# Kernel optimization log

Measured on AMD Instinct MI355X. Metric: run time of the kernel, lower is better.

Reference implementation:

```python
import jax, jax.numpy as jnp
import numpy as np
import math

CHUNK = 64

def _linear(x, W, b):
    # torch nn.Linear: y = x @ W.T + b
    return jnp.einsum('bsd,ed->bse', x, W) + b

def setup_inputs() -> dict:
    key = jax.random.key(0)
    ks = jax.random.split(key, 10)
    B, S, D = 4, 4096, 512
    scale = 0.02
    inp = {
        'x': jax.random.normal(ks[0], (B, S, D), jnp.float32),
        'base_phases': jax.random.normal(ks[1], (S, D), jnp.float32) * math.pi,
        'Wk': jax.random.normal(ks[2], (D, D), jnp.float32) * scale,
        'bk': jnp.zeros((D,), jnp.float32),
        'Wv': jax.random.normal(ks[3], (D, D), jnp.float32) * scale,
        'bv': jnp.zeros((D,), jnp.float32),
        'Wq': jax.random.normal(ks[4], (D, D), jnp.float32) * scale,
        'bq': jnp.zeros((D,), jnp.float32),
        'Wkm': jax.random.normal(ks[5], (D, D), jnp.float32) * scale,
        'bkm': jnp.zeros((D,), jnp.float32),
        'Wqm': jax.random.normal(ks[6], (D, D), jnp.float32) * scale,
        'bqm': jnp.zeros((D,), jnp.float32),
        'mod_scale': jnp.ones((1,), jnp.float32) * 0.1,
        'ln_g': jnp.ones((D,), jnp.float32),
        'ln_b': jnp.zeros((D,), jnp.float32),
        'Wo': jax.random.normal(ks[7], (D, D), jnp.float32) * scale,
        'bo': jnp.zeros((D,), jnp.float32),
    }
    return inp

def reference(x, base_phases, Wk, bk, Wv, bv, Wq, bq, Wkm, bkm, Wqm, bqm, mod_scale, ln_g, ln_b, Wo, bo):
    B, S, D = x.shape
    bp = base_phases[:S][None]                      # [1,S,D]
    key = _linear(x, Wk, bk)
    value = _linear(x, Wv, bv)
    query = _linear(x, Wq, bq)
    key_phase = bp + _linear(key, Wkm, bkm) * mod_scale
    query_phase = bp + _linear(query, Wqm, bqm) * mod_scale
    bound_real = value * jnp.cos(key_phase)
    bound_imag = value * jnp.sin(key_phase)
    # chunked cumulative memory (S divisible by CHUNK -> no padding)
    nC = S // CHUNK
    br = bound_real.reshape(B, nC, CHUNK, D)
    bi = bound_imag.reshape(B, nC, CHUNK, D)
    qp = query_phase.reshape(B, nC, CHUNK, D)
    mem_real = jnp.cumsum(br, axis=2)
    mem_imag = jnp.cumsum(bi, axis=2)
    retrieved = (mem_real * jnp.cos(qp) + mem_imag * jnp.sin(qp)).reshape(B, S, D)
    retrieved = retrieved / math.sqrt(D)
    # LayerNorm + Linear (to_out)
    mu = jnp.mean(retrieved, axis=-1, keepdims=True)
    var = jnp.mean((retrieved - mu) ** 2, axis=-1, keepdims=True)
    normed = (retrieved - mu) / jnp.sqrt(var + 1e-5) * ln_g + ln_b
    out = _linear(normed, Wo, bo)
    return x + out
```

## Files before the change

kernel.cpp:

```cpp
#include <hip/hip_runtime.h>
#include <hip/hip_bf16.h>


typedef __attribute__((ext_vector_type(8))) short short8;
typedef __attribute__((ext_vector_type(4))) float f32x4;

#define M_TOK   16384
#define DIM     512
#define NCHUNK  64
#define RPAD    520

__device__ __forceinline__ void gll16(const void* g, void* l) {
  __builtin_amdgcn_global_load_lds(
      (const __attribute__((address_space(1))) unsigned int*)g,
      (__attribute__((address_space(3))) unsigned int*)l, 16, 0, 0);
}

__device__ __forceinline__ uint2 pack4bf(float4 v) {
  union { __hip_bfloat16 h[4]; uint2 u; } t;
  t.h[0] = __float2bfloat16(v.x);
  t.h[1] = __float2bfloat16(v.y);
  t.h[2] = __float2bfloat16(v.z);
  t.h[3] = __float2bfloat16(v.w);
  return t.u;
}

__global__ __launch_bounds__(256) void prep_all(
    const float* __restrict__ x, __hip_bfloat16* __restrict__ x_bf,
    const float* __restrict__ Wv, const float* __restrict__ Wo,
    const float* __restrict__ bv,
    const float* __restrict__ Wkm, const float* __restrict__ Wqm,
    const float* __restrict__ Wk, const float* __restrict__ Wq,
    const float* __restrict__ bk, const float* __restrict__ bkm,
    const float* __restrict__ bq, const float* __restrict__ bqm,
    __hip_bfloat16* __restrict__ Wall, float* __restrict__ bc1,
    __hip_bfloat16* __restrict__ Wm_bf, __hip_bfloat16* __restrict__ WT_bf) {
  const int tid = threadIdx.x;
  if (blockIdx.x < 8192) {
    int i = blockIdx.x * 256 + tid;
    ((uint2*)x_bf)[i] = pack4bf(((const float4*)x)[i]);
    return;
  }
  const int b = blockIdx.x - 8192;
  if (b < 512) {
    int m = b >> 8;
    int idx = ((b & 255) * 256 + tid) * 4;
    const float* src = m ? Wo : Wv;
    __hip_bfloat16* dst = Wall + (m ? (size_t)1536 * 512 : 0);
    ((uint2*)dst)[idx >> 2] = pack4bf(*(const float4*)(src + idx));
    int t = b * 256 + tid;
    if (t < 512) bc1[t] = bv[t];
  } else if (b < 1024) {
    int bb = b - 512;
    int m = bb >> 8;
    int idx = ((bb & 255) * 256 + tid) * 4;
    const float* src = m ? Wqm : Wkm;
    ((uint2*)(Wm_bf + (size_t)m * 262144))[idx >> 2] =
        pack4bf(*(const float4*)(src + idx));
  } else if (b < 1152) {
    __shared__ float tile[64][65];
    int bb = b - 1024;
    int z = bb >> 6;
    int tl = bb & 63;
    int tr = tl >> 3, tc = tl & 7;
    const float* src = z ? Wq : Wk;
#pragma unroll
    for (int i = 0; i < 4; i++) {
      int r = (tid >> 4) + 16 * i;
      int c4 = (tid & 15) * 4;
      float4 v = *(const float4*)(src + (size_t)(tr * 64 + r) * 512 +
                                  tc * 64 + c4);
      tile[r][c4 + 0] = v.x;
      tile[r][c4 + 1] = v.y;
      tile[r][c4 + 2] = v.z;
      tile[r][c4 + 3] = v.w;
    }
    __syncthreads();
    int orow = tid >> 2;
    int seg = tid & 3;
    __hip_bfloat16* dst = WT_bf + (size_t)z * 262144 +
                          (size_t)(tc * 64 + orow) * 512 + tr * 64 + seg * 16;
#pragma unroll
    for (int q = 0; q < 4; q++) {
      float4 v;
      v.x = tile[seg * 16 + q * 4 + 0][orow];
      v.y = tile[seg * 16 + q * 4 + 1][orow];
      v.z = tile[seg * 16 + q * 4 + 2][orow];
      v.w = tile[seg * 16 + q * 4 + 3][orow];
      *(uint2*)(dst + q * 4) = pack4bf(v);
    }
  } else {
    int row = (b - 1152) * 4 + (tid >> 6);
    int lane = tid & 63;
    int z = row >> 9;
    int i = row & 511;
    const float* Wm = z ? Wqm : Wkm;
    const float* b0 = z ? bq : bk;
    const float* bm = z ? bqm : bkm;
    const float4* w4 = (const float4*)(Wm + (size_t)i * 512 + lane * 8);
    const float4* v4 = (const float4*)(b0 + lane * 8);
    float4 w0 = w4[0], w1 = w4[1], c0 = v4[0], c1 = v4[1];
    float acc = w0.x * c0.x + w0.y * c0.y + w0.z * c0.z + w0.w * c0.w +
                w1.x * c1.x + w1.y * c1.y + w1.z * c1.z + w1.w * c1.w;
#pragma unroll
    for (int off = 32; off; off >>= 1) acc += __shfl_xor(acc, off, 64);
    if (lane == 0) bc1[512 + z * 512 + i] = acc + bm[i];
  }
}

__global__ __launch_bounds__(256) void gemm_bt(
    const __hip_bfloat16* __restrict__ A, int lda,
    const __hip_bfloat16* __restrict__ Bt,
    const float* __restrict__ bias,
    __hip_bfloat16* __restrict__ Cout, int ldc) {
  constexpr int K = 512, BK = 32;
  __shared__ __align__(16) __hip_bfloat16 As[128 * BK];
  __shared__ __align__(16) __hip_bfloat16 Bs[128 * BK];

  const int tid  = threadIdx.x;
  const int lane = tid & 63;
  const int w    = tid >> 6;
  const int wm   = w >> 1;
  const int wn   = w & 1;
  const int m0   = blockIdx.y * 128;
  const int n0   = blockIdx.x * 128;

  const int rS0    = (w * 2 + 0) * 16 + (lane >> 2);
  const int rS1    = (w * 2 + 1) * 16 + (lane >> 2);
  const int kInRow = (lane & 3) * 8;
  const __hip_bfloat16* gA0 = A + (size_t)(m0 + rS0) * lda + kInRow;
  const __hip_bfloat16* gA1 = A + (size_t)(m0 + rS1) * lda + kInRow;
  const __hip_bfloat16* gB0 = Bt + (size_t)(n0 + rS0) * K + kInRow;
  const __hip_bfloat16* gB1 = Bt + (size_t)(n0 + rS1) * K + kInRow;
  char* ldsA0 = (char*)As + (w * 2 + 0) * 1024;
  char* ldsA1 = (char*)As + (w * 2 + 1) * 1024;
  char* ldsB0 = (char*)Bs + (w * 2 + 0) * 1024;
  char* ldsB1 = (char*)Bs + (w * 2 + 1) * 1024;

  f32x4 acc[4][4] = {};

  const int rfA = lane & 15;
  const int rfK = (lane >> 4) * 8;

  for (int kt = 0; kt < K; kt += BK) {
    __syncthreads();
    gll16(gA0 + kt, ldsA0);
    gll16(gA1 + kt, ldsA1);
    gll16(gB0 + kt, ldsB0);
    gll16(gB1 + kt, ldsB1);
    __syncthreads();

    short8 af[4], bf[4];
#pragma unroll
    for (int i = 0; i < 4; i++)
      af[i] = *(const short8*)(As + (wm * 64 + i * 16 + rfA) * BK + rfK);
#pragma unroll
    for (int j = 0; j < 4; j++)
      bf[j] = *(const short8*)(Bs + (wn * 64 + j * 16 + rfA) * BK + rfK);
#pragma unroll
    for (int i = 0; i < 4; i++)
#pragma unroll
      for (int j = 0; j < 4; j++)
        acc[i][j] = __builtin_amdgcn_mfma_f32_16x16x32_bf16(
            af[i], bf[j], acc[i][j], 0, 0, 0);
  }

  const int cq = lane >> 4;
#pragma unroll
  for (int i = 0; i < 4; i++) {
    int row = m0 + wm * 64 + i * 16 + cq * 4;
#pragma unroll
    for (int j = 0; j < 4; j++) {
      int col = n0 + wn * 64 + j * 16 + (lane & 15);
      float bz = bias[col];
#pragma unroll
      for (int r = 0; r < 4; r++) {
        float v = acc[i][j][r] + bz;
        Cout[(size_t)(row + r) * ldc + col] = __float2bfloat16(v);
      }
    }
  }
}

__global__ __launch_bounds__(256) void gemm_compose(
    const __hip_bfloat16* __restrict__ Wm_bf,
    const __hip_bfloat16* __restrict__ WT_bf,
    __hip_bfloat16* __restrict__ Wall) {
  constexpr int K = 512, BK = 32;
  const __hip_bfloat16* A  = Wm_bf + (size_t)blockIdx.z * 262144;
  const __hip_bfloat16* Bt = WT_bf + (size_t)blockIdx.z * 262144;
  __hip_bfloat16* C = Wall + (size_t)(512 + blockIdx.z * 512) * 512;
  __shared__ __align__(16) __hip_bfloat16 As[128 * BK];
  __shared__ __align__(16) __hip_bfloat16 Bs[128 * BK];

  const int tid  = threadIdx.x;
  const int lane = tid & 63;
  const int w    = tid >> 6;
  const int wm   = w >> 1;
  const int wn   = w & 1;
  const int m0   = blockIdx.y * 128;
  const int n0   = blockIdx.x * 128;

  const int rS0    = (w * 2 + 0) * 16 + (lane >> 2);
  const int rS1    = (w * 2 + 1) * 16 + (lane >> 2);
  const int kInRow = (lane & 3) * 8;
  const __hip_bfloat16* gA0 = A + (size_t)(m0 + rS0) * K + kInRow;
  const __hip_bfloat16* gA1 = A + (size_t)(m0 + rS1) * K + kInRow;
  const __hip_bfloat16* gB0 = Bt + (size_t)(n0 + rS0) * K + kInRow;
  const __hip_bfloat16* gB1 = Bt + (size_t)(n0 + rS1) * K + kInRow;
  char* ldsA0 = (char*)As + (w * 2 + 0) * 1024;
  char* ldsA1 = (char*)As + (w * 2 + 1) * 1024;
  char* ldsB0 = (char*)Bs + (w * 2 + 0) * 1024;
  char* ldsB1 = (char*)Bs + (w * 2 + 1) * 1024;

  f32x4 acc[4][4] = {};
  const int rfA = lane & 15;
  const int rfK = (lane >> 4) * 8;

  for (int kt = 0; kt < K; kt += BK) {
    __syncthreads();
    gll16(gA0 + kt, ldsA0);
    gll16(gA1 + kt, ldsA1);
    gll16(gB0 + kt, ldsB0);
    gll16(gB1 + kt, ldsB1);
    __syncthreads();

    short8 af[4], bf[4];
#pragma unroll
    for (int i = 0; i < 4; i++)
      af[i] = *(const short8*)(As + (wm * 64 + i * 16 + rfA) * BK + rfK);
#pragma unroll
    for (int j = 0; j < 4; j++)
      bf[j] = *(const short8*)(Bs + (wn * 64 + j * 16 + rfA) * BK + rfK);
#pragma unroll
    for (int i = 0; i < 4; i++)
#pragma unroll
      for (int j = 0; j < 4; j++)
        acc[i][j] = __builtin_amdgcn_mfma_f32_16x16x32_bf16(
            af[i], bf[j], acc[i][j], 0, 0, 0);
  }

  const int cq = lane >> 4;
#pragma unroll
  for (int i = 0; i < 4; i++) {
    int row = m0 + wm * 64 + i * 16 + cq * 4;
#pragma unroll
    for (int j = 0; j < 4; j++) {
      int col = n0 + wn * 64 + j * 16 + (lane & 15);
#pragma unroll
      for (int r = 0; r < 4; r++)
        C[(size_t)(row + r) * 512 + col] = __float2bfloat16(acc[i][j][r]);
    }
  }
}

__global__ __launch_bounds__(1024) void fused_pg(
    const __hip_bfloat16* __restrict__ VKQ,
    const float* __restrict__ bp,
    const float* __restrict__ mod_scale,
    const float* __restrict__ ln_g, const float* __restrict__ ln_b,
    const __hip_bfloat16* __restrict__ WoB,
    const float* __restrict__ bo,
    const float* __restrict__ x,
    float* __restrict__ out) {
  __shared__ __hip_bfloat16 R[64 * RPAD];
  __shared__ float Tr[512], Ti[512];
  const int tid    = threadIdx.x;
  const int seg    = tid >> 9;
  const int d      = tid & 511;
  const int blk    = blockIdx.x;
  const int token0 = blk * 64;
  const int sg0    = (blk & (NCHUNK - 1)) * 64;
  const float msc  = mod_scale[0];
  const float isd  = 0.044194173824159216f;

  {
    const int s0 = seg * 32;
    float mr = 0.f, mi = 0.f;
    const __hip_bfloat16* vb = VKQ + (size_t)(token0 + s0) * 1536 + d;
    const float* bb = bp + (size_t)(sg0 + s0) * 512 + d;
#pragma unroll 4
    for (int s = 0; s < 32; ++s) {
      float v  = __bfloat162float(vb[(size_t)s * 1536]);
      float km = __bfloat162float(vb[(size_t)s * 1536 + 512]);
      float qm = __bfloat162float(vb[(size_t)s * 1536 + 1024]);
      float b  = bb[(size_t)s * 512];
      float kp = b + km * msc;
      float qp = b + qm * msc;
      float sk, ck, sq, cq;
      __sincosf(kp, &sk, &ck);
      __sincosf(qp, &sq, &cq);
      mr += v * ck;
      mi += v * sk;
      R[(s0 + s) * RPAD + d] = __float2bfloat16((mr * cq + mi * sq) * isd);
    }
    if (seg == 0) {
      Tr[d] = mr;
      Ti[d] = mi;
    }
  }
  __syncthreads();

  {
    const int r0 = 32 + seg * 16;
    const float pr = Tr[d] * isd;
    const float pi = Ti[d] * isd;
    const __hip_bfloat16* qb = VKQ + (size_t)(token0 + r0) * 1536 + 1024 + d;
    const float* bb = bp + (size_t)(sg0 + r0) * 512 + d;
#pragma unroll 4
    for (int s = 0; s < 16; ++s) {
      float qm = __bfloat162float(qb[(size_t)s * 1536]);
      float b  = bb[(size_t)s * 512];
      float qp = b + qm * msc;
      float sq, cq;
      __sincosf(qp, &sq, &cq);
      int idx = (r0 + s) * RPAD + d;
      float v = __bfloat162float(R[idx]) + pr * cq + pi * sq;
      R[idx] = __float2bfloat16(v);
    }
  }
  __syncthreads();

  {
    const int lane = tid & 63;
    const int wv   = tid >> 6;
    float gj[8], bj[8];
#pragma unroll
    for (int j = 0; j < 8; j++) {
      int col = lane + 64 * j;
      gj[j] = ln_g[col];
      bj[j] = ln_b[col];
    }
    for (int rr = 0; rr < 4; ++rr) {
      int row = wv * 4 + rr;
      float vals[8], sum = 0.f, sq2 = 0.f;
#pragma unroll
      for (int j = 0; j < 8; j++) {
        float v = __bfloat162float(R[row * RPAD + lane + 64 * j]);
        vals[j] = v;
        sum += v;
        sq2 += v * v;
      }
#pragma unroll
      for (int off = 32; off; off >>= 1) {
        sum += __shfl_xor(sum, off, 64);
        sq2 += __shfl_xor(sq2, off, 64);
      }
      float mu   = sum * (1.f / 512.f);
      float var  = sq2 * (1.f / 512.f) - mu * mu;
      float rstd = rsqrtf(var + 1e-5f);
#pragma unroll
      for (int j = 0; j < 8; j++) {
        float nv = (vals[j] - mu) * rstd * gj[j] + bj[j];
        R[row * RPAD + lane + 64 * j] = __float2bfloat16(nv);
      }
    }
  }
  __syncthreads();

  {
    const int lane = tid & 63;
    const int w    = tid >> 6;
    const int rfA  = lane & 15;
    const int rfK  = (lane >> 4) * 8;
    f32x4 acc[4][2] = {};

    for (int kt = 0; kt < 512; kt += 32) {
      short8 af[4], bf[2];
#pragma unroll
      for (int j = 0; j < 2; j++) {
        int col = w * 32 + j * 16 + rfA;
        bf[j] = *(const short8*)(WoB + (size_t)col * 512 + kt + rfK);
      }
#pragma unroll
      for (int i = 0; i < 4; i++)
        af[i] = *(const short8*)(R + (i * 16 + rfA) * RPAD + kt + rfK);
#pragma unroll
      for (int i = 0; i < 4; i++)
#pragma unroll
        for (int j = 0; j < 2; j++)
          acc[i][j] = __builtin_amdgcn_mfma_f32_16x16x32_bf16(
              af[i], bf[j], acc[i][j], 0, 0, 0);
    }

    const int cq = lane >> 4;
    float bz[2];
#pragma unroll
    for (int j = 0; j < 2; j++) bz[j] = bo[w * 32 + j * 16 + (lane & 15)];
#pragma unroll
    for (int i = 0; i < 4; i++) {
      int row = token0 + i * 16 + cq * 4;
#pragma unroll
      for (int j = 0; j < 2; j++) {
        int col = w * 32 + j * 16 + (lane & 15);
#pragma unroll
        for (int r = 0; r < 4; r++) {
          size_t o = (size_t)(row + r) * 512 + col;
          out[o] = acc[i][j][r] + bz[j] + x[o];
        }
      }
    }
  }
}

extern "C" void kernel_launch(void* const* d_in, const int* in_sizes, int n_in,
                              void* d_out, int out_size, void* d_ws,
                              size_t ws_size, hipStream_t stream) {
  const float* x    = (const float*)d_in[0];
  const float* bp   = (const float*)d_in[1];
  const float* Wk   = (const float*)d_in[2];
  const float* bk   = (const float*)d_in[3];
  const float* Wv   = (const float*)d_in[4];
  const float* bv   = (const float*)d_in[5];
  const float* Wq   = (const float*)d_in[6];
  const float* bq   = (const float*)d_in[7];
  const float* Wkm  = (const float*)d_in[8];
  const float* bkm  = (const float*)d_in[9];
  const float* Wqm  = (const float*)d_in[10];
  const float* bqm  = (const float*)d_in[11];
  const float* msc  = (const float*)d_in[12];
  const float* lng  = (const float*)d_in[13];
  const float* lnb  = (const float*)d_in[14];
  const float* Wo   = (const float*)d_in[15];
  const float* bo   = (const float*)d_in[16];
  float* out = (float*)d_out;

  char* ws = (char*)d_ws;
  __hip_bfloat16* x_bf  = (__hip_bfloat16*)ws;  ws += (size_t)M_TOK * DIM * 2;
  __hip_bfloat16* Wall  = (__hip_bfloat16*)ws;  ws += (size_t)2048 * 512 * 2;
  __hip_bfloat16* Wm_bf = (__hip_bfloat16*)ws;  ws += (size_t)2 * 262144 * 2;
  __hip_bfloat16* WT_bf = (__hip_bfloat16*)ws;  ws += (size_t)2 * 262144 * 2;
  float*          bc1   = (float*)ws;           ws += 1536 * 4;
  __hip_bfloat16* VKQ   = (__hip_bfloat16*)ws;  ws += (size_t)M_TOK * 1536 * 2;

  prep_all<<<9600, 256, 0, stream>>>(x, x_bf, Wv, Wo, bv, Wkm, Wqm, Wk, Wq,
                                     bk, bkm, bq, bqm, Wall, bc1, Wm_bf,
                                     WT_bf);
  gemm_compose<<<dim3(4, 4, 2), 256, 0, stream>>>(Wm_bf, WT_bf, Wall);
  gemm_bt<<<dim3(12, 128), 256, 0, stream>>>(x_bf, DIM, Wall, bc1, VKQ, 1536);
  fused_pg<<<256, 1024, 0, stream>>>(VKQ, bp, msc, lng, lnb,
                                     Wall + (size_t)1536 * 512, bo, x, out);
}
```

Before: 206.5 us.

## Double-buffer LDS tiles in gemm_bt and remap blocks for XCD L2 locality

Splits the bf16 projection GEMM's shared-memory tiles into two buffers. The global-to-LDS loads for the next K-step are issued before the MFMAs on the current step, so one barrier per iteration replaces two and load latency can overlap compute. It also launches a 1D grid and remaps block IDs so each group of 8-strided blocks gets a contiguous tile range, aiming for better L2 reuse per XCD. This doubles LDS use per block, which may reduce occupancy. The overlap only happens if the compiler does not insert a full vmcnt wait before the LDS reads.

```diff
diff --git a/kernel.cpp b/kernel.cpp
--- a/kernel.cpp
+++ b/kernel.cpp
@@ -114,16 +114,19 @@
     const float* __restrict__ bias,
     __hip_bfloat16* __restrict__ Cout, int ldc) {
   constexpr int K = 512, BK = 32;
-  __shared__ __align__(16) __hip_bfloat16 As[128 * BK];
-  __shared__ __align__(16) __hip_bfloat16 Bs[128 * BK];
+  __shared__ __align__(16) __hip_bfloat16 As[2][128 * BK];
+  __shared__ __align__(16) __hip_bfloat16 Bs[2][128 * BK];
 
   const int tid  = threadIdx.x;
   const int lane = tid & 63;
   const int w    = tid >> 6;
   const int wm   = w >> 1;
   const int wn   = w & 1;
-  const int m0   = blockIdx.y * 128;
-  const int n0   = blockIdx.x * 128;
+  const int lb = (blockIdx.x & 7) * 192 + (blockIdx.x >> 3);
+  const int by = lb / 12;
+  const int bx = lb - by * 12;
+  const int m0 = by * 128;
+  const int n0 = bx * 128;
 
   const int rS0    = (w * 2 + 0) * 16 + (lane >> 2);
   const int rS1    = (w * 2 + 1) * 16 + (lane >> 2);
@@ -132,37 +135,49 @@
   const __hip_bfloat16* gA1 = A + (size_t)(m0 + rS1) * lda + kInRow;
   const __hip_bfloat16* gB0 = Bt + (size_t)(n0 + rS0) * K + kInRow;
   const __hip_bfloat16* gB1 = Bt + (size_t)(n0 + rS1) * K + kInRow;
-  char* ldsA0 = (char*)As + (w * 2 + 0) * 1024;
-  char* ldsA1 = (char*)As + (w * 2 + 1) * 1024;
-  char* ldsB0 = (char*)Bs + (w * 2 + 0) * 1024;
-  char* ldsB1 = (char*)Bs + (w * 2 + 1) * 1024;
+  char* ldsA0 = (char*)&As[0][0] + (w * 2 + 0) * 1024;
+  char* ldsA1 = (char*)&As[0][0] + (w * 2 + 1) * 1024;
+  char* ldsB0 = (char*)&Bs[0][0] + (w * 2 + 0) * 1024;
+  char* ldsB1 = (char*)&Bs[0][0] + (w * 2 + 1) * 1024;
 
   f32x4 acc[4][4] = {};
 
   const int rfA = lane & 15;
   const int rfK = (lane >> 4) * 8;
 
+  gll16(gA0, ldsA0);
+  gll16(gA1, ldsA1);
+  gll16(gB0, ldsB0);
+  gll16(gB1, ldsB1);
+
+#pragma unroll 2
   for (int kt = 0; kt < K; kt += BK) {
+    const int cur = (kt >> 5) & 1;
+    const int coff = cur * 8192;
     __syncthreads();
-    gll16(gA0 + kt, ldsA0);
-    gll16(gA1 + kt, ldsA1);
-    gll16(gB0 + kt, ldsB0);
-    gll16(gB1 + kt, ldsB1);
-    __syncthreads();
-
-    short8 af[4], bf[4];
+    const int nxt = kt + BK;
+    if (nxt < K) {
+      const int noff = 8192 - coff;
+      gll16(gA0 + nxt, ldsA0 + noff);
+      gll16(gA1 + nxt, ldsA1 + noff);
+      gll16(gB0 + nxt, ldsB0 + noff);
+      gll16(gB1 + nxt, ldsB1 + noff);
+    }
+    const __hip_bfloat16* Ah = &As[cur][0];
+    const __hip_bfloat16* Bh = &Bs[cur][0];
+    short8 af[4], bfv[4];
 #pragma unroll
     for (int i = 0; i < 4; i++)
-      af[i] = *(const short8*)(As + (wm * 64 + i * 16 + rfA) * BK + rfK);
+      af[i] = *(const short8*)(Ah + (wm * 64 + i * 16 + rfA) * BK + rfK);
 #pragma unroll
     for (int j = 0; j < 4; j++)
-      bf[j] = *(const short8*)(Bs + (wn * 64 + j * 16 + rfA) * BK + rfK);
+      bfv[j] = *(const short8*)(Bh + (wn * 64 + j * 16 + rfA) * BK + rfK);
 #pragma unroll
     for (int i = 0; i < 4; i++)
 #pragma unroll
       for (int j = 0; j < 4; j++)
         acc[i][j] = __builtin_amdgcn_mfma_f32_16x16x32_bf16(
-            af[i], bf[j], acc[i][j], 0, 0, 0);
+            af[i], bfv[j], acc[i][j], 0, 0, 0);
   }
 
   const int cq = lane >> 4;
@@ -437,7 +452,7 @@
                                      bk, bkm, bq, bqm, Wall, bc1, Wm_bf,
                                      WT_bf);
   gemm_compose<<<dim3(4, 4, 2), 256, 0, stream>>>(Wm_bf, WT_bf, Wall);
-  gemm_bt<<<dim3(12, 128), 256, 0, stream>>>(x_bf, DIM, Wall, bc1, VKQ, 1536);
+  gemm_bt<<<dim3(1536), 256, 0, stream>>>(x_bf, DIM, Wall, bc1, VKQ, 1536);
   fused_pg<<<256, 1024, 0, stream>>>(VKQ, bp, msc, lng, lnb,
                                      Wall + (size_t)1536 * 512, bo, x, out);
 }
```

Result: no change. 206.6 us (+0.0%).
